# Performance work log

Measured on AMD Instinct MI355X. Metric: run time of the kernel, lower is better.

Reference implementation:

```python
import jax, jax.numpy as jnp
import numpy as np

B, S, H, NH, DIS = 8, 512, 512, 8, 32
HD = H // NH  # head_dim = 64


def setup_inputs() -> dict:
    key = jax.random.key(0)
    ks = jax.random.split(key, 9)
    sc = 0.05
    return {
        "x": jax.random.normal(ks[0], (B, S, H), jnp.float32),
        "rel_distance": jax.random.randint(ks[1], (B, S, 2 * S), 0, DIS, jnp.int64),
        "mask": jnp.zeros((B, S, 2 * S), jnp.bool_),
        "query_pos_embedding": jax.random.normal(ks[2], (DIS, H), jnp.float32) * sc,
        "key_pos_embedding": jax.random.normal(ks[3], (DIS, H), jnp.float32) * sc,
        "value_pos_embedding": jax.random.normal(ks[4], (DIS, H), jnp.float32) * sc,
        "Wq": jax.random.normal(ks[5], (H, H), jnp.float32) * sc,
        "Wk": jax.random.normal(ks[6], (2 * H, H), jnp.float32) * sc,
        "Wv": jax.random.normal(ks[7], (2 * H, H), jnp.float32) * sc,
        "Wo": jax.random.normal(ks[8], (H, H), jnp.float32) * sc,
    }


def reference(x, rel_distance, mask, query_pos_embedding, key_pos_embedding,
              value_pos_embedding, Wq, Wk, Wv, Wo):
    b, s, _ = x.shape
    scale = jnp.sqrt(jnp.asarray(HD, x.dtype))

    # projections (torch Linear: y = x @ W.T)
    q = (x @ Wq.T).reshape(b, s, NH, HD).transpose(0, 2, 1, 3)        # [B,h,S,d]
    k = (x @ Wk.T).reshape(b, 2 * s, NH, HD).transpose(0, 2, 1, 3)    # [B,h,2S,d]
    v = (x @ Wv.T).reshape(b, 2 * s, NH, HD).transpose(0, 2, 1, 3)    # [B,h,2S,d]

    rel = jnp.broadcast_to(rel_distance[:, None], (b, NH, s, 2 * s))  # [B,h,S,2S]

    # relative-position weights via gather along distance axis
    q_emb = query_pos_embedding.reshape(DIS, NH, HD)                  # [n,h,d]
    qpw_full = jnp.einsum('bhsd,nhd->bhsn', q, q_emb)                 # [B,h,S,n]
    qpw = jnp.take_along_axis(qpw_full, rel, axis=3)                  # [B,h,S,2S]

    k_emb = key_pos_embedding.reshape(DIS, NH, HD)
    kpw_full = jnp.einsum('bhkd,nhd->bhkn', k, k_emb)                 # [B,h,2S,n]
    kpw = jnp.take_along_axis(kpw_full, rel.transpose(0, 1, 3, 2), axis=3)  # [B,h,2S,S]
    kpw = kpw.transpose(0, 1, 3, 2)                                   # [B,h,S,2S]

    scores = (jnp.einsum('bhsd,bhkd->bhsk', q, k) + qpw + kpw) / scale
    scores = jnp.where(mask[:, None], -jnp.inf, scores)
    probs = jax.nn.softmax(scores, axis=-1)                           # [B,h,S,2S]

    # scatter-add probs into distance buckets: [B,h,S,n]
    bi = jnp.arange(b)[:, None, None, None]
    hi = jnp.arange(NH)[None, :, None, None]
    si = jnp.arange(s)[None, None, :, None]
    vdw = jnp.zeros((b, NH, s, DIS), probs.dtype).at[bi, hi, si, rel].add(probs)

    v_emb = value_pos_embedding.reshape(DIS, NH, HD)                  # [n,h,d]
    out = jnp.einsum('bhsk,bhkd->bhsd', probs, v) \
        + jnp.einsum('bhsn,nhd->bhsd', vdw, v_emb)                    # [B,h,S,d]
    out = out.transpose(0, 2, 1, 3).reshape(b, s, H)
    return out @ Wo.T
```

## Files before the change

kernel.cpp:

```cpp
#include <hip/hip_runtime.h>
#include <math.h>

#define Bc 8
#define Sc 512
#define Hc 512
#define NHc 8
#define HDc 64
#define DISc 32
#define S2c 1024

typedef __attribute__((ext_vector_type(8))) short bf16x8;
typedef __attribute__((ext_vector_type(4))) float f32x4;
#define MFMA16(a, b, c) __builtin_amdgcn_mfma_f32_16x16x32_bf16(a, b, c, 0, 0, 0)

__device__ __forceinline__ unsigned short f2bf(float f) {
  unsigned u = __float_as_uint(f);
  return (unsigned short)((u + 0x7fffu + ((u >> 16) & 1u)) >> 16);
}
__device__ __forceinline__ float b2f(unsigned short u) {
  return __uint_as_float((unsigned)u << 16);
}
__device__ __forceinline__ bf16x8 ldb16x8(const unsigned short* p) {
  union { uint4 u; bf16x8 s; } cv;
  cv.u = *(const uint4*)p;
  return cv.s;
}

__global__ __launch_bounds__(256) void cvt5_k(
    const float* __restrict__ x, const float* __restrict__ wq,
    const float* __restrict__ wk, const float* __restrict__ wv,
    const float* __restrict__ wo, unsigned short* __restrict__ x16,
    unsigned short* __restrict__ w16q, unsigned short* __restrict__ w16k,
    unsigned short* __restrict__ w16v, unsigned short* __restrict__ w16o) {
  int i = blockIdx.x * 256 + threadIdx.x;
  const float* src; unsigned short* dst; int off; float sc = 1.f;
  if (i < 524288)      { src = x;  dst = x16;  off = i; }
  else if (i < 589824) { src = wq; dst = w16q; off = i - 524288; sc = 0.125f; }
  else if (i < 720896) { src = wk; dst = w16k; off = i - 589824; }
  else if (i < 851968) { src = wv; dst = w16v; off = i - 720896; }
  else                 { src = wo; dst = w16o; off = i - 851968; }
  float4 v = ((const float4*)src)[off];
  ushort4 u;
  u.x = f2bf(v.x * sc); u.y = f2bf(v.y * sc);
  u.z = f2bf(v.z * sc); u.w = f2bf(v.w * sc);
  ((ushort4*)dst)[off] = u;
}

__global__ __launch_bounds__(256) void pack_k(const int* __restrict__ rel,
                                              const unsigned char* __restrict__ mask,
                                              unsigned char* __restrict__ pk8) {
  int i = blockIdx.x * 256 + threadIdx.x;
  const int* rp = rel + i * 16;
  uint4 mu = *(const uint4*)(mask + i * 16);
  const unsigned char* mb = (const unsigned char*)&mu;
  uint4 o;
  unsigned* ow = (unsigned*)&o;
#pragma unroll
  for (int g = 0; g < 4; ++g) {
    int4 r4 = ((const int4*)rp)[g];
    unsigned b0 = ((unsigned)r4.x & 31u) | (mb[g * 4 + 0] ? 0x80u : 0u);
    unsigned b1 = ((unsigned)r4.y & 31u) | (mb[g * 4 + 1] ? 0x80u : 0u);
    unsigned b2 = ((unsigned)r4.z & 31u) | (mb[g * 4 + 2] ? 0x80u : 0u);
    unsigned b3 = ((unsigned)r4.w & 31u) | (mb[g * 4 + 3] ? 0x80u : 0u);
    ow[g] = b0 | (b1 << 8) | (b2 << 16) | (b3 << 24);
  }
  *(uint4*)(pk8 + i * 16) = o;
}

__global__ __launch_bounds__(256) void wemb_k(
    const float* __restrict__ qpe, const float* __restrict__ kpe,
    const float* __restrict__ Wq, const float* __restrict__ Wk,
    unsigned short* __restrict__ wqp, unsigned short* __restrict__ wkp) {
  const int bid = blockIdx.x;
  const int cc = bid & 3, unit = bid >> 2;
  const int c0 = cc << 7;
  const int t = threadIdx.x;
  const float* emb; const float* Wsrc; unsigned short* outp; int rowbase, h;
  if (unit < 8) {
    h = unit; emb = qpe; Wsrc = Wq + (size_t)(h * 64) * 512; outp = wqp; rowbase = h * 32;
  } else {
    int u = unit - 8; int e = u >> 3; h = u & 7;
    emb = kpe; Wsrc = Wk + (size_t)(e * 512 + h * 64) * 512; outp = wkp;
    rowbase = e * 256 + h * 32;
  }
  __shared__ float es[32][65];
  __shared__ float wsh[64][132];
  {
    int n = t >> 3, d4 = (t & 7) << 3;
    float4 v0 = *(const float4*)(emb + (size_t)n * 512 + h * 64 + d4);
    float4 v1 = *(const float4*)(emb + (size_t)n * 512 + h * 64 + d4 + 4);
    *(float4*)&es[n][d4] = v0;
    *(float4*)&es[n][d4 + 4] = v1;
  }
#pragma unroll
  for (int p = 0; p < 8; ++p) {
    int slot = t + (p << 8);
    int d = slot >> 5, c4 = (slot & 31) << 2;
    *(float4*)&wsh[d][c4] = *(const float4*)(Wsrc + (size_t)d * 512 + c0 + c4);
  }
  __syncthreads();
  const int n = t >> 3, cb = (t & 7) << 4;
  float acc[16] = {};
#pragma unroll
  for (int d = 0; d < 64; ++d) {
    float ev = es[n][d];
    float4 w0 = *(const float4*)&wsh[d][cb];
    float4 w1 = *(const float4*)&wsh[d][cb + 4];
    float4 w2 = *(const float4*)&wsh[d][cb + 8];
    float4 w3 = *(const float4*)&wsh[d][cb + 12];
    acc[0] = fmaf(ev, w0.x, acc[0]);   acc[1] = fmaf(ev, w0.y, acc[1]);
    acc[2] = fmaf(ev, w0.z, acc[2]);   acc[3] = fmaf(ev, w0.w, acc[3]);
    acc[4] = fmaf(ev, w1.x, acc[4]);   acc[5] = fmaf(ev, w1.y, acc[5]);
    acc[6] = fmaf(ev, w1.z, acc[6]);   acc[7] = fmaf(ev, w1.w, acc[7]);
    acc[8] = fmaf(ev, w2.x, acc[8]);   acc[9] = fmaf(ev, w2.y, acc[9]);
    acc[10] = fmaf(ev, w2.z, acc[10]); acc[11] = fmaf(ev, w2.w, acc[11]);
    acc[12] = fmaf(ev, w3.x, acc[12]); acc[13] = fmaf(ev, w3.y, acc[13]);
    acc[14] = fmaf(ev, w3.z, acc[14]); acc[15] = fmaf(ev, w3.w, acc[15]);
  }
  unsigned short* orow = outp + (size_t)(rowbase + n) * 512 + c0 + cb;
#pragma unroll
  for (int j = 0; j < 16; ++j) orow[j] = f2bf(acc[j] * 0.125f);
}

template <int MODE>
__global__ __launch_bounds__(256, 4) void gemm16_k(
    const unsigned short* __restrict__ A, const unsigned short* __restrict__ B1,
    const unsigned short* __restrict__ B2, void* __restrict__ out1,
    void* __restrict__ out2, int M, int N, int K, int nsplit) {
  const int t = threadIdx.x;
  const int w = t >> 6, lane = t & 63, ln = lane & 15, qd = lane >> 4;
  const int wm = (w >> 1) << 5, wn = (w & 1) << 5;
  const int m0 = blockIdx.y << 6, n0 = blockIdx.x << 6;
  __shared__ unsigned short As[64 * 72];
  __shared__ unsigned short Bs[64 * 72];
  const bool reg1 = (n0 < nsplit);
  const unsigned short* Bb =
      reg1 ? B1 + (size_t)n0 * K : B2 + (size_t)(n0 - nsplit) * K;
  const int r0 = t >> 3, c8 = (t & 7) << 3;
  const unsigned short* ga = A + (size_t)(m0 + r0) * K + c8;
  const unsigned short* gb = Bb + (size_t)r0 * K + c8;
  const size_t half = (size_t)32 * K;
  uint4 va0 = *(const uint4*)ga, va1 = *(const uint4*)(ga + half);
  uint4 vb0 = *(const uint4*)gb, vb1 = *(const uint4*)(gb + half);
  f32x4 z = {0.f, 0.f, 0.f, 0.f};
  f32x4 acc[2][2] = {{z, z}, {z, z}};
  for (int k0 = 0; k0 < K; k0 += 64) {
    *(uint4*)&As[r0 * 72 + c8] = va0;
    *(uint4*)&As[(r0 + 32) * 72 + c8] = va1;
    *(uint4*)&Bs[r0 * 72 + c8] = vb0;
    *(uint4*)&Bs[(r0 + 32) * 72 + c8] = vb1;
    __syncthreads();
    if (k0 + 64 < K) {
      va0 = *(const uint4*)(ga + k0 + 64);
      va1 = *(const uint4*)(ga + half + k0 + 64);
      vb0 = *(const uint4*)(gb + k0 + 64);
      vb1 = *(const uint4*)(gb + half + k0 + 64);
    }
#pragma unroll
    for (int kk = 0; kk < 64; kk += 32) {
      bf16x8 a0 = ldb16x8(&As[(wm + ln) * 72 + kk + qd * 8]);
      bf16x8 a1 = ldb16x8(&As[(wm + 16 + ln) * 72 + kk + qd * 8]);
      bf16x8 b0 = ldb16x8(&Bs[(wn + ln) * 72 + kk + qd * 8]);
      bf16x8 b1 = ldb16x8(&Bs[(wn + 16 + ln) * 72 + kk + qd * 8]);
      acc[0][0] = MFMA16(a0, b0, acc[0][0]);
      acc[0][1] = MFMA16(a0, b1, acc[0][1]);
      acc[1][0] = MFMA16(a1, b0, acc[1][0]);
      acc[1][1] = MFMA16(a1, b1, acc[1][1]);
    }
    __syncthreads();
  }
#pragma unroll
  for (int tm = 0; tm < 2; ++tm)
#pragma unroll
    for (int tn = 0; tn < 2; ++tn)
#pragma unroll
      for (int r = 0; r < 4; ++r) {
        int m = m0 + wm + tm * 16 + qd * 4 + r;
        int n = n0 + wn + tn * 16 + ln;
        float v = acc[tm][tn][r];
        int bb = m >> 9, s = m & 511;
        if (MODE == 0) {
          ((float*)out1)[(size_t)m * N + n] = v;
        } else if (MODE == 3) {
          int e = n >> 9, hh = (n >> 6) & 7, d = n & 63;
          int k2 = 2 * s + e;
          ((unsigned short*)out1)[((size_t)(bb * 8 + hh) * 64 + d) * 1024 + k2] = f2bf(v);
        } else if (MODE == 1) {
          if (reg1) {
            int hh = (n >> 6) & 7, d = n & 63;
            ((unsigned short*)out1)[((size_t)(bb * 8 + hh) * 512 + s) * 64 + d] = f2bf(v);
          } else {
            int n2 = n - 512, hh = n2 >> 5, nn = n2 & 31;
            ((unsigned short*)out2)[((size_t)(bb * 8 + hh) * 512 + s) * 32 + nn] = f2bf(v);
          }
        } else {
          if (reg1) {
            int e = n >> 9, hh = (n >> 6) & 7, d = n & 63;
            int k2 = 2 * s + e;
            ((unsigned short*)out1)[((size_t)(bb * 8 + hh) * 1024 + k2) * 64 + d] = f2bf(v);
          } else {
            int n2 = n - 1024, e = n2 >> 8, hh = (n2 >> 5) & 7, nn = n2 & 31;
            int k2 = 2 * s + e;
            ((unsigned short*)out2)[((size_t)(bb * 8 + hh) * 1024 + k2) * 32 + nn] = f2bf(v);
          }
        }
      }
}

__global__ __launch_bounds__(512, 4) void attn6_k(
    const unsigned short* __restrict__ q16h, const unsigned short* __restrict__ kb16,
    const unsigned short* __restrict__ vT16, const unsigned short* __restrict__ qpw16,
    const unsigned short* __restrict__ kpw16, const unsigned char* __restrict__ pk8,
    const float* __restrict__ v_emb, unsigned short* __restrict__ attn16) {
  const int bid = blockIdx.x;
  const int b = bid & 7;
  const int h = (bid >> 3) & 7;
  const int qb = ((bid >> 6) & 7) << 6;
  const int t = threadIdx.x;
  const int w = t >> 6;
  const int g = w >> 2;
  const int ws4 = w & 3;
  const int lane = t & 63;
  const int ln = lane & 15;
  const int qd = lane >> 4;

  __shared__ __align__(16) char smem[60928];
  unsigned char*  pkt  = (unsigned char*)smem;
  unsigned short* kpws = (unsigned short*)(smem + 10240);
  unsigned short* q32s = (unsigned short*)(smem + 19456);
  unsigned short* pbuf = (unsigned short*)(smem + 24064);
  unsigned long long* vdwm64 = (unsigned long long*)(smem + 42496);
  float*          accbuf = (float*)smem;
  unsigned short* vest   = (unsigned short*)(smem + 24064);
  unsigned short* vdwb   = (unsigned short*)(smem + 29184);

  for (int i = t; i < 4 * 16 * 36; i += 512) vdwm64[i] = 0ull;
  if (t < 256) {
    int row = t >> 2, c8 = (t & 3) << 3;
    *(uint4*)&q32s[row * 36 + c8] =
        *(const uint4*)(qpw16 + ((size_t)((b * 8 + h) * 512 + qb) + row) * 32 + c8);
  }
  const unsigned short* kbase = kb16 + (size_t)(b * 8 + h) * 65536;
  const unsigned short* vbase = vT16 + (size_t)(b * 8 + h) * 65536;
  bf16x8 aQ[2];
  {
    const unsigned short* qsrc =
        q16h + ((size_t)((b * 8 + h) * 512 + qb + ws4 * 16 + ln)) * 64;
    aQ[0] = ldb16x8(qsrc + qd * 8);
    aQ[1] = ldb16x8(qsrc + 32 + qd * 8);
  }
  f32x4 z = {0.f, 0.f, 0.f, 0.f};
  f32x4 acc[4] = {z, z, z, z};

  const int u = t & 255, gg = t >> 8;
  const int qr = u >> 2, cg = (u & 3) << 4;
  const int kc8 = (u & 3) << 3;
  const unsigned char* pks = pk8 + ((size_t)(b * 512 + qb + qr)) * 1024 + (gg << 9);
  const unsigned short* kps =
      kpw16 + ((size_t)((b * 8 + h) * 1024) + (gg << 9) + qr) * 32 + kc8;
  unsigned char* pt_w = pkt + gg * 5120 + qr * 80 + cg;
  unsigned short* kp_w = kpws + gg * 2304 + qr * 36 + kc8;

  uint4 pv = *(const uint4*)(pks + cg);
  uint4 kv = *(const uint4*)kps;

  for (int kti = 0; kti < 8; ++kti) {
    *(uint4*)pt_w = pv;
    *(uint4*)kp_w = kv;
    __syncthreads();
    if (kti < 7) {
      pv = *(const uint4*)(pks + ((kti + 1) << 6) + cg);
      kv = *(const uint4*)(kps + ((size_t)(kti + 1) << 11));
    }
    const int kt0 = (kti + g * 8) << 6;

    f32x4 sc4[4];
#pragma unroll
    for (int t4 = 0; t4 < 4; ++t4) {
      f32x4 c = z;
      c = MFMA16(aQ[0], ldb16x8(kbase + (size_t)(kt0 + t4 * 16 + ln) * 64 + qd * 8), c);
      c = MFMA16(aQ[1], ldb16x8(kbase + (size_t)(kt0 + t4 * 16 + ln) * 64 + 32 + qd * 8), c);
      sc4[t4] = c;
    }

    unsigned char* pt_ = pkt + g * 5120;
    unsigned short* kp_ = kpws + g * 2304;
#pragma unroll
    for (int r = 0; r < 4; ++r) {
#pragma unroll
      for (int t4 = 0; t4 < 4; ++t4) {
        int row_l = ws4 * 16 + qd * 4 + r;
        int kl = t4 * 16 + ln;
        unsigned um = pt_[row_l * 80 + kl];
        int rd = um & 31;
        float s = sc4[t4][r] + b2f(q32s[row_l * 36 + rd]) + b2f(kp_[kl * 36 + rd]);
        float p = (um & 0x80u) ? 0.f : __expf(s);
        atomicAdd(&vdwm64[ws4 * 576 + (qd * 4 + r) * 36 + rd],
                  (unsigned long long)(p * 67108864.0f));
        pbuf[w * 1152 + (qd * 4 + r) * 72 + kl] = f2bf(p);
      }
    }

    bf16x8 a0 = ldb16x8(&pbuf[w * 1152 + ln * 72 + qd * 8]);
    bf16x8 a1 = ldb16x8(&pbuf[w * 1152 + ln * 72 + 32 + qd * 8]);
#pragma unroll
    for (int dt = 0; dt < 4; ++dt) {
      acc[dt] = MFMA16(a0, ldb16x8(vbase + (size_t)(dt * 16 + ln) * 1024 + kt0 + qd * 8), acc[dt]);
      acc[dt] = MFMA16(a1, ldb16x8(vbase + (size_t)(dt * 16 + ln) * 1024 + kt0 + 32 + qd * 8), acc[dt]);
    }
    __syncthreads();
  }

  if (t < 256) {
    int n = t >> 3, d0 = (t & 7) << 3;
    const float* src = v_emb + ((size_t)n << 9) + (h << 6) + d0;
    float4 f0 = *(const float4*)src;
    float4 f1 = *(const float4*)(src + 4);
    vest[(d0 + 0) * 40 + n] = f2bf(f0.x); vest[(d0 + 1) * 40 + n] = f2bf(f0.y);
    vest[(d0 + 2) * 40 + n] = f2bf(f0.z); vest[(d0 + 3) * 40 + n] = f2bf(f0.w);
    vest[(d0 + 4) * 40 + n] = f2bf(f1.x); vest[(d0 + 5) * 40 + n] = f2bf(f1.y);
    vest[(d0 + 6) * 40 + n] = f2bf(f1.z); vest[(d0 + 7) * 40 + n] = f2bf(f1.w);
  } else {
    int row = lane >> 2, n0 = (lane & 3) << 3;
    float vv[8];
#pragma unroll
    for (int j = 0; j < 8; ++j)
      vv[j] = (float)vdwm64[ws4 * 576 + row * 36 + n0 + j] * 1.4901161193847656e-8f;
    ushort4 u0, u1;
    u0.x = f2bf(vv[0]); u0.y = f2bf(vv[1]); u0.z = f2bf(vv[2]); u0.w = f2bf(vv[3]);
    u1.x = f2bf(vv[4]); u1.y = f2bf(vv[5]); u1.z = f2bf(vv[6]); u1.w = f2bf(vv[7]);
    *(ushort4*)&vdwb[ws4 * 640 + row * 40 + n0] = u0;
    *(ushort4*)&vdwb[ws4 * 640 + row * 40 + n0 + 4] = u1;
  }
  __syncthreads();

  if (g == 1) {
    bf16x8 av = ldb16x8(&vdwb[ws4 * 640 + ln * 40 + qd * 8]);
#pragma unroll
    for (int dt = 0; dt < 4; ++dt)
      acc[dt] = MFMA16(av, ldb16x8(&vest[(dt * 16 + ln) * 40 + qd * 8]), acc[dt]);
#pragma unroll
    for (int r = 0; r < 4; ++r)
#pragma unroll
      for (int dt = 0; dt < 4; ++dt)
        accbuf[ws4 * 1088 + (qd * 4 + r) * 68 + dt * 16 + ln] = acc[dt][r];
  }
  __syncthreads();

  if (g == 0) {
    float inv[4];
#pragma unroll
    for (int r = 0; r < 4; ++r) {
      unsigned long long lu = 0ull;
#pragma unroll
      for (int n = 0; n < 32; ++n)
        lu += vdwm64[ws4 * 576 + (qd * 4 + r) * 36 + n];
      inv[r] = 67108864.0f / (float)lu;
    }
    unsigned short* obase =
        attn16 + ((size_t)(b * 512 + qb + ws4 * 16 + qd * 4)) * 512 + (h << 6);
#pragma unroll
    for (int r = 0; r < 4; ++r)
#pragma unroll
      for (int dt = 0; dt < 4; ++dt) {
        float v = (acc[dt][r] + accbuf[ws4 * 1088 + (qd * 4 + r) * 68 + dt * 16 + ln]) * inv[r];
        obase[(size_t)r * 512 + dt * 16 + ln] = f2bf(v);
      }
  }
}

extern "C" void kernel_launch(void* const* d_in, const int* in_sizes, int n_in,
                              void* d_out, int out_size, void* d_ws, size_t ws_size,
                              hipStream_t stream) {
  const float* x = (const float*)d_in[0];
  const int* rel = (const int*)d_in[1];
  const unsigned char* mask = (const unsigned char*)d_in[2];
  const float* qpe = (const float*)d_in[3];
  const float* kpe = (const float*)d_in[4];
  const float* vpe = (const float*)d_in[5];
  const float* Wq = (const float*)d_in[6];
  const float* Wk = (const float*)d_in[7];
  const float* Wv = (const float*)d_in[8];
  const float* Wo = (const float*)d_in[9];
  float* out = (float*)d_out;

  unsigned short* u = (unsigned short*)d_ws;
  unsigned short* x16    = u;
  unsigned short* w16q   = x16 + 2097152;
  unsigned short* w16k   = w16q + 262144;
  unsigned short* w16v   = w16k + 524288;
  unsigned short* w16o   = w16v + 524288;
  unsigned short* wqp16  = w16o + 262144;
  unsigned short* wkp16  = wqp16 + 131072;
  unsigned short* q16h   = wkp16 + 262144;
  unsigned short* qpw16  = q16h + 2097152;
  unsigned short* kb16   = qpw16 + 1048576;
  unsigned short* kpw16  = kb16 + 4194304;
  unsigned short* vT16   = kpw16 + 2097152;
  unsigned short* attn16 = vT16 + 4194304;
  unsigned char* pk8 = (unsigned char*)(attn16 + 2097152);

  pack_k<<<1024, 256, 0, stream>>>(rel, mask, pk8);
  cvt5_k<<<3584, 256, 0, stream>>>(x, Wq, Wk, Wv, Wo, x16, w16q, w16k, w16v, w16o);
  wemb_k<<<96, 256, 0, stream>>>(qpe, kpe, Wq, Wk, wqp16, wkp16);
  gemm16_k<1><<<dim3(12, 64), 256, 0, stream>>>(x16, w16q, wqp16, q16h, qpw16,
                                                4096, 768, 512, 512);
  gemm16_k<2><<<dim3(24, 64), 256, 0, stream>>>(x16, w16k, wkp16, kb16, kpw16,
                                                4096, 1536, 512, 1024);
  gemm16_k<3><<<dim3(16, 64), 256, 0, stream>>>(x16, w16v, nullptr, vT16, nullptr,
                                                4096, 1024, 512, 1024);
  attn6_k<<<512, 512, 0, stream>>>(q16h, kb16, vT16, qpw16, kpw16, pk8, vpe, attn16);
  gemm16_k<0><<<dim3(8, 64), 256, 0, stream>>>(attn16, w16o, nullptr, out, nullptr,
                                               4096, 512, 512, 512);
}
```

Baseline: 221.2 us.

## Use direct global-to-LDS loads and 128x64 tiles in bf16 GEMM

The projection and output GEMMs now stage tiles with global_load_lds, which copies global memory straight into LDS instead of going through registers, and the block tile grows from 64x64 to 128x64 with four row-fragments per wave. The goal is less register traffic for staging and more MFMA reuse per LDS fragment load. The cost is that the register prefetch of the next K tile is gone, the LDS padding is dropped (which may cause bank conflicts on fragment reads), and the grids launch half as many blocks.

```diff
diff --git a/kernel.cpp b/kernel.cpp
--- a/kernel.cpp
+++ b/kernel.cpp
@@ -24,6 +24,11 @@
   union { uint4 u; bf16x8 s; } cv;
   cv.u = *(const uint4*)p;
   return cv.s;
+}
+__device__ __forceinline__ void gll16(const unsigned short* g, void* l) {
+  __builtin_amdgcn_global_load_lds(
+      (const __attribute__((address_space(1))) unsigned int*)g,
+      (__attribute__((address_space(3))) unsigned int*)l, 16, 0, 0);
 }
 
 __global__ __launch_bounds__(256) void cvt5_k(
@@ -129,48 +134,47 @@
     void* __restrict__ out2, int M, int N, int K, int nsplit) {
   const int t = threadIdx.x;
   const int w = t >> 6, lane = t & 63, ln = lane & 15, qd = lane >> 4;
-  const int wm = (w >> 1) << 5, wn = (w & 1) << 5;
-  const int m0 = blockIdx.y << 6, n0 = blockIdx.x << 6;
-  __shared__ unsigned short As[64 * 72];
-  __shared__ unsigned short Bs[64 * 72];
+  const int wm = (w >> 1) << 6, wn = (w & 1) << 5;
+  const int m0 = blockIdx.y << 7, n0 = blockIdx.x << 6;
+  __shared__ __align__(16) unsigned short As[128 * 64];
+  __shared__ __align__(16) unsigned short Bs[64 * 64];
   const bool reg1 = (n0 < nsplit);
   const unsigned short* Bb =
       reg1 ? B1 + (size_t)n0 * K : B2 + (size_t)(n0 - nsplit) * K;
-  const int r0 = t >> 3, c8 = (t & 7) << 3;
-  const unsigned short* ga = A + (size_t)(m0 + r0) * K + c8;
-  const unsigned short* gb = Bb + (size_t)r0 * K + c8;
-  const size_t half = (size_t)32 * K;
-  uint4 va0 = *(const uint4*)ga, va1 = *(const uint4*)(ga + half);
-  uint4 vb0 = *(const uint4*)gb, vb1 = *(const uint4*)(gb + half);
+  const int lr = lane >> 3, lc = (lane & 7) << 3;
+  const unsigned short* ga = A + (size_t)(m0 + (w << 5) + lr) * K + lc;
+  const unsigned short* gb = Bb + (size_t)((w << 4) + lr) * K + lc;
+  char* lA = (char*)As + (w << 12);
+  char* lB = (char*)Bs + (w << 11);
   f32x4 z = {0.f, 0.f, 0.f, 0.f};
-  f32x4 acc[2][2] = {{z, z}, {z, z}};
+  f32x4 acc[4][2] = {{z, z}, {z, z}, {z, z}, {z, z}};
   for (int k0 = 0; k0 < K; k0 += 64) {
-    *(uint4*)&As[r0 * 72 + c8] = va0;
-    *(uint4*)&As[(r0 + 32) * 72 + c8] = va1;
-    *(uint4*)&Bs[r0 * 72 + c8] = vb0;
-    *(uint4*)&Bs[(r0 + 32) * 72 + c8] = vb1;
+#pragma unroll
+    for (int i = 0; i < 4; ++i)
+      gll16(ga + (size_t)(i << 3) * K + k0, lA + (i << 10));
+#pragma unroll
+    for (int i = 0; i < 2; ++i)
+      gll16(gb + (size_t)(i << 3) * K + k0, lB + (i << 10));
     __syncthreads();
-    if (k0 + 64 < K) {
-      va0 = *(const uint4*)(ga + k0 + 64);
-      va1 = *(const uint4*)(ga + half + k0 + 64);
-      vb0 = *(const uint4*)(gb + k0 + 64);
-      vb1 = *(const uint4*)(gb + half + k0 + 64);
-    }
 #pragma unroll
     for (int kk = 0; kk < 64; kk += 32) {
-      bf16x8 a0 = ldb16x8(&As[(wm + ln) * 72 + kk + qd * 8]);
-      bf16x8 a1 = ldb16x8(&As[(wm + 16 + ln) * 72 + kk + qd * 8]);
-      bf16x8 b0 = ldb16x8(&Bs[(wn + ln) * 72 + kk + qd * 8]);
-      bf16x8 b1 = ldb16x8(&Bs[(wn + 16 + ln) * 72 + kk + qd * 8]);
-      acc[0][0] = MFMA16(a0, b0, acc[0][0]);
-      acc[0][1] = MFMA16(a0, b1, acc[0][1]);
-      acc[1][0] = MFMA16(a1, b0, acc[1][0]);
-      acc[1][1] = MFMA16(a1, b1, acc[1][1]);
+      bf16x8 af[4], bfr[2];
+#pragma unroll
+      for (int x = 0; x < 4; ++x)
+        af[x] = ldb16x8(&As[(wm + x * 16 + ln) * 64 + kk + qd * 8]);
+#pragma unroll
+      for (int y = 0; y < 2; ++y)
+        bfr[y] = ldb16x8(&Bs[(wn + y * 16 + ln) * 64 + kk + qd * 8]);
+#pragma unroll
+      for (int tm = 0; tm < 4; ++tm)
+#pragma unroll
+        for (int tn = 0; tn < 2; ++tn)
+          acc[tm][tn] = MFMA16(af[tm], bfr[tn], acc[tm][tn]);
     }
     __syncthreads();
   }
 #pragma unroll
-  for (int tm = 0; tm < 2; ++tm)
+  for (int tm = 0; tm < 4; ++tm)
 #pragma unroll
     for (int tn = 0; tn < 2; ++tn)
 #pragma unroll
@@ -403,13 +407,13 @@
   pack_k<<<1024, 256, 0, stream>>>(rel, mask, pk8);
   cvt5_k<<<3584, 256, 0, stream>>>(x, Wq, Wk, Wv, Wo, x16, w16q, w16k, w16v, w16o);
   wemb_k<<<96, 256, 0, stream>>>(qpe, kpe, Wq, Wk, wqp16, wkp16);
-  gemm16_k<1><<<dim3(12, 64), 256, 0, stream>>>(x16, w16q, wqp16, q16h, qpw16,
+  gemm16_k<1><<<dim3(12, 32), 256, 0, stream>>>(x16, w16q, wqp16, q16h, qpw16,
                                                 4096, 768, 512, 512);
-  gemm16_k<2><<<dim3(24, 64), 256, 0, stream>>>(x16, w16k, wkp16, kb16, kpw16,
+  gemm16_k<2><<<dim3(24, 32), 256, 0, stream>>>(x16, w16k, wkp16, kb16, kpw16,
                                                 4096, 1536, 512, 1024);
-  gemm16_k<3><<<dim3(16, 64), 256, 0, stream>>>(x16, w16v, nullptr, vT16, nullptr,
+  gemm16_k<3><<<dim3(16, 32), 256, 0, stream>>>(x16, w16v, nullptr, vT16, nullptr,
                                                 4096, 1024, 512, 1024);
   attn6_k<<<512, 512, 0, stream>>>(q16h, kb16, vT16, qpw16, kpw16, pk8, vpe, attn16);
-  gemm16_k<0><<<dim3(8, 64), 256, 0, stream>>>(attn16, w16o, nullptr, out, nullptr,
+  gemm16_k<0><<<dim3(8, 32), 256, 0, stream>>>(attn16, w16o, nullptr, out, nullptr,
                                                4096, 512, 512, 512);
 }
```

After: 231.0 us. 1.04x slower.

## Merge Q/K/V projection GEMMs into one launch and shrink attention P buffer

Applied to the files above, without the earlier changes.

The three projection GEMM launches (Q+qpw, K+kpw, V transposed) become one kernel over a 52-column-tile grid that selects the weight source and output layout per tile. This removes two launch gaps and gives one larger wave of blocks. The attention kernel now handles the P·V product in two 32-key halves, so the per-wave probability buffer shrinks and total LDS drops. Launch bounds rise to 6 blocks per SM to raise occupancy, which may cost registers or spill.

```diff
diff --git a/kernel.cpp b/kernel.cpp
--- a/kernel.cpp
+++ b/kernel.cpp
@@ -122,35 +122,41 @@
   for (int j = 0; j < 16; ++j) orow[j] = f2bf(acc[j] * 0.125f);
 }
 
-template <int MODE>
-__global__ __launch_bounds__(256, 4) void gemm16_k(
-    const unsigned short* __restrict__ A, const unsigned short* __restrict__ B1,
-    const unsigned short* __restrict__ B2, void* __restrict__ out1,
-    void* __restrict__ out2, int M, int N, int K, int nsplit) {
+__global__ __launch_bounds__(256, 4) void gemmqkv_k(
+    const unsigned short* __restrict__ A,
+    const unsigned short* __restrict__ wq, const unsigned short* __restrict__ wqp,
+    const unsigned short* __restrict__ wk, const unsigned short* __restrict__ wkp,
+    const unsigned short* __restrict__ wv,
+    unsigned short* __restrict__ q16h, unsigned short* __restrict__ qpw16,
+    unsigned short* __restrict__ kb16, unsigned short* __restrict__ kpw16,
+    unsigned short* __restrict__ vT16) {
   const int t = threadIdx.x;
   const int w = t >> 6, lane = t & 63, ln = lane & 15, qd = lane >> 4;
   const int wm = (w >> 1) << 5, wn = (w & 1) << 5;
   const int m0 = blockIdx.y << 6, n0 = blockIdx.x << 6;
   __shared__ unsigned short As[64 * 72];
   __shared__ unsigned short Bs[64 * 72];
-  const bool reg1 = (n0 < nsplit);
-  const unsigned short* Bb =
-      reg1 ? B1 + (size_t)n0 * K : B2 + (size_t)(n0 - nsplit) * K;
+  const unsigned short* Bb;
+  if (n0 < 512)        Bb = wq  + (size_t)n0 * 512;
+  else if (n0 < 768)   Bb = wqp + (size_t)(n0 - 512) * 512;
+  else if (n0 < 1792)  Bb = wk  + (size_t)(n0 - 768) * 512;
+  else if (n0 < 2304)  Bb = wkp + (size_t)(n0 - 1792) * 512;
+  else                 Bb = wv  + (size_t)(n0 - 2304) * 512;
   const int r0 = t >> 3, c8 = (t & 7) << 3;
-  const unsigned short* ga = A + (size_t)(m0 + r0) * K + c8;
-  const unsigned short* gb = Bb + (size_t)r0 * K + c8;
-  const size_t half = (size_t)32 * K;
+  const unsigned short* ga = A + (size_t)(m0 + r0) * 512 + c8;
+  const unsigned short* gb = Bb + (size_t)r0 * 512 + c8;
+  const size_t half = (size_t)32 * 512;
   uint4 va0 = *(const uint4*)ga, va1 = *(const uint4*)(ga + half);
   uint4 vb0 = *(const uint4*)gb, vb1 = *(const uint4*)(gb + half);
   f32x4 z = {0.f, 0.f, 0.f, 0.f};
   f32x4 acc[2][2] = {{z, z}, {z, z}};
-  for (int k0 = 0; k0 < K; k0 += 64) {
+  for (int k0 = 0; k0 < 512; k0 += 64) {
     *(uint4*)&As[r0 * 72 + c8] = va0;
     *(uint4*)&As[(r0 + 32) * 72 + c8] = va1;
     *(uint4*)&Bs[r0 * 72 + c8] = vb0;
     *(uint4*)&Bs[(r0 + 32) * 72 + c8] = vb1;
     __syncthreads();
-    if (k0 + 64 < K) {
+    if (k0 + 64 < 512) {
       va0 = *(const uint4*)(ga + k0 + 64);
       va1 = *(const uint4*)(ga + half + k0 + 64);
       vb0 = *(const uint4*)(gb + k0 + 64);
@@ -177,37 +183,86 @@
       for (int r = 0; r < 4; ++r) {
         int m = m0 + wm + tm * 16 + qd * 4 + r;
         int n = n0 + wn + tn * 16 + ln;
-        float v = acc[tm][tn][r];
+        unsigned short v16 = f2bf(acc[tm][tn][r]);
         int bb = m >> 9, s = m & 511;
-        if (MODE == 0) {
-          ((float*)out1)[(size_t)m * N + n] = v;
-        } else if (MODE == 3) {
-          int e = n >> 9, hh = (n >> 6) & 7, d = n & 63;
+        if (n0 < 512) {
+          int hh = (n >> 6) & 7, d = n & 63;
+          q16h[((size_t)(bb * 8 + hh) * 512 + s) * 64 + d] = v16;
+        } else if (n0 < 768) {
+          int n2 = n - 512, hh = n2 >> 5, nn = n2 & 31;
+          qpw16[((size_t)(bb * 8 + hh) * 512 + s) * 32 + nn] = v16;
+        } else if (n0 < 1792) {
+          int n2 = n - 768, e = n2 >> 9, hh = (n2 >> 6) & 7, d = n2 & 63;
           int k2 = 2 * s + e;
-          ((unsigned short*)out1)[((size_t)(bb * 8 + hh) * 64 + d) * 1024 + k2] = f2bf(v);
-        } else if (MODE == 1) {
-          if (reg1) {
-            int hh = (n >> 6) & 7, d = n & 63;
-            ((unsigned short*)out1)[((size_t)(bb * 8 + hh) * 512 + s) * 64 + d] = f2bf(v);
-          } else {
-            int n2 = n - 512, hh = n2 >> 5, nn = n2 & 31;
-            ((unsigned short*)out2)[((size_t)(bb * 8 + hh) * 512 + s) * 32 + nn] = f2bf(v);
-          }
+          kb16[((size_t)(bb * 8 + hh) * 1024 + k2) * 64 + d] = v16;
+        } else if (n0 < 2304) {
+          int n2 = n - 1792, e = n2 >> 8, hh = (n2 >> 5) & 7, nn = n2 & 31;
+          int k2 = 2 * s + e;
+          kpw16[((size_t)(bb * 8 + hh) * 1024 + k2) * 32 + nn] = v16;
         } else {
-          if (reg1) {
-            int e = n >> 9, hh = (n >> 6) & 7, d = n & 63;
-            int k2 = 2 * s + e;
-            ((unsigned short*)out1)[((size_t)(bb * 8 + hh) * 1024 + k2) * 64 + d] = f2bf(v);
-          } else {
-            int n2 = n - 1024, e = n2 >> 8, hh = (n2 >> 5) & 7, nn = n2 & 31;
-            int k2 = 2 * s + e;
-            ((unsigned short*)out2)[((size_t)(bb * 8 + hh) * 1024 + k2) * 32 + nn] = f2bf(v);
-          }
+          int n2 = n - 2304, e = n2 >> 9, hh = (n2 >> 6) & 7, d = n2 & 63;
+          int k2 = 2 * s + e;
+          vT16[((size_t)(bb * 8 + hh) * 64 + d) * 1024 + k2] = v16;
         }
       }
 }
 
-__global__ __launch_bounds__(512, 4) void attn6_k(
+__global__ __launch_bounds__(256, 4) void gemmo_k(
+    const unsigned short* __restrict__ A, const unsigned short* __restrict__ Bw,
+    float* __restrict__ out) {
+  const int t = threadIdx.x;
+  const int w = t >> 6, lane = t & 63, ln = lane & 15, qd = lane >> 4;
+  const int wm = (w >> 1) << 5, wn = (w & 1) << 5;
+  const int m0 = blockIdx.y << 6, n0 = blockIdx.x << 6;
+  __shared__ unsigned short As[64 * 72];
+  __shared__ unsigned short Bs[64 * 72];
+  const unsigned short* Bb = Bw + (size_t)n0 * 512;
+  const int r0 = t >> 3, c8 = (t & 7) << 3;
+  const unsigned short* ga = A + (size_t)(m0 + r0) * 512 + c8;
+  const unsigned short* gb = Bb + (size_t)r0 * 512 + c8;
+  const size_t half = (size_t)32 * 512;
+  uint4 va0 = *(const uint4*)ga, va1 = *(const uint4*)(ga + half);
+  uint4 vb0 = *(const uint4*)gb, vb1 = *(const uint4*)(gb + half);
+  f32x4 z = {0.f, 0.f, 0.f, 0.f};
+  f32x4 acc[2][2] = {{z, z}, {z, z}};
+  for (int k0 = 0; k0 < 512; k0 += 64) {
+    *(uint4*)&As[r0 * 72 + c8] = va0;
+    *(uint4*)&As[(r0 + 32) * 72 + c8] = va1;
+    *(uint4*)&Bs[r0 * 72 + c8] = vb0;
+    *(uint4*)&Bs[(r0 + 32) * 72 + c8] = vb1;
+    __syncthreads();
+    if (k0 + 64 < 512) {
+      va0 = *(const uint4*)(ga + k0 + 64);
+      va1 = *(const uint4*)(ga + half + k0 + 64);
+      vb0 = *(const uint4*)(gb + k0 + 64);
+      vb1 = *(const uint4*)(gb + half + k0 + 64);
+    }
+#pragma unroll
+    for (int kk = 0; kk < 64; kk += 32) {
+      bf16x8 a0 = ldb16x8(&As[(wm + ln) * 72 + kk + qd * 8]);
+      bf16x8 a1 = ldb16x8(&As[(wm + 16 + ln) * 72 + kk + qd * 8]);
+      bf16x8 b0 = ldb16x8(&Bs[(wn + ln) * 72 + kk + qd * 8]);
+      bf16x8 b1 = ldb16x8(&Bs[(wn + 16 + ln) * 72 + kk + qd * 8]);
+      acc[0][0] = MFMA16(a0, b0, acc[0][0]);
+      acc[0][1] = MFMA16(a0, b1, acc[0][1]);
+      acc[1][0] = MFMA16(a1, b0, acc[1][0]);
+      acc[1][1] = MFMA16(a1, b1, acc[1][1]);
+    }
+    __syncthreads();
+  }
+#pragma unroll
+  for (int tm = 0; tm < 2; ++tm)
+#pragma unroll
+    for (int tn = 0; tn < 2; ++tn)
+#pragma unroll
+      for (int r = 0; r < 4; ++r) {
+        int m = m0 + wm + tm * 16 + qd * 4 + r;
+        int n = n0 + wn + tn * 16 + ln;
+        out[(size_t)m * 512 + n] = acc[tm][tn][r];
+      }
+}
+
+__global__ __launch_bounds__(512, 6) void attn6_k(
     const unsigned short* __restrict__ q16h, const unsigned short* __restrict__ kb16,
     const unsigned short* __restrict__ vT16, const unsigned short* __restrict__ qpw16,
     const unsigned short* __restrict__ kpw16, const unsigned char* __restrict__ pk8,
@@ -224,15 +279,15 @@
   const int ln = lane & 15;
   const int qd = lane >> 4;
 
-  __shared__ __align__(16) char smem[60928];
+  __shared__ __align__(16) char smem[52736];
   unsigned char*  pkt  = (unsigned char*)smem;
   unsigned short* kpws = (unsigned short*)(smem + 10240);
   unsigned short* q32s = (unsigned short*)(smem + 19456);
   unsigned short* pbuf = (unsigned short*)(smem + 24064);
-  unsigned long long* vdwm64 = (unsigned long long*)(smem + 42496);
+  unsigned long long* vdwm64 = (unsigned long long*)(smem + 34304);
   float*          accbuf = (float*)smem;
-  unsigned short* vest   = (unsigned short*)(smem + 24064);
-  unsigned short* vdwb   = (unsigned short*)(smem + 29184);
+  unsigned short* vest   = (unsigned short*)(smem + 19456);
+  unsigned short* vdwb   = (unsigned short*)(smem + 24576);
 
   for (int i = t; i < 4 * 16 * 36; i += 512) vdwm64[i] = 0ull;
   if (t < 256) {
@@ -286,27 +341,27 @@
     unsigned char* pt_ = pkt + g * 5120;
     unsigned short* kp_ = kpws + g * 2304;
 #pragma unroll
-    for (int r = 0; r < 4; ++r) {
-#pragma unroll
-      for (int t4 = 0; t4 < 4; ++t4) {
-        int row_l = ws4 * 16 + qd * 4 + r;
-        int kl = t4 * 16 + ln;
-        unsigned um = pt_[row_l * 80 + kl];
-        int rd = um & 31;
-        float s = sc4[t4][r] + b2f(q32s[row_l * 36 + rd]) + b2f(kp_[kl * 36 + rd]);
-        float p = (um & 0x80u) ? 0.f : __expf(s);
-        atomicAdd(&vdwm64[ws4 * 576 + (qd * 4 + r) * 36 + rd],
-                  (unsigned long long)(p * 67108864.0f));
-        pbuf[w * 1152 + (qd * 4 + r) * 72 + kl] = f2bf(p);
+    for (int hf = 0; hf < 2; ++hf) {
+#pragma unroll
+      for (int r = 0; r < 4; ++r) {
+#pragma unroll
+        for (int t4h = 0; t4h < 2; ++t4h) {
+          int t4 = hf * 2 + t4h;
+          int row_l = ws4 * 16 + qd * 4 + r;
+          int kl = t4 * 16 + ln;
+          unsigned um = pt_[row_l * 80 + kl];
+          int rd = um & 31;
+          float s = sc4[t4][r] + b2f(q32s[row_l * 36 + rd]) + b2f(kp_[kl * 36 + rd]);
+          float p = (um & 0x80u) ? 0.f : __expf(s);
+          atomicAdd(&vdwm64[ws4 * 576 + (qd * 4 + r) * 36 + rd],
+                    (unsigned long long)(p * 67108864.0f));
+          pbuf[w * 640 + (qd * 4 + r) * 40 + t4h * 16 + ln] = f2bf(p);
+        }
       }
-    }
-
-    bf16x8 a0 = ldb16x8(&pbuf[w * 1152 + ln * 72 + qd * 8]);
-    bf16x8 a1 = ldb16x8(&pbuf[w * 1152 + ln * 72 + 32 + qd * 8]);
-#pragma unroll
-    for (int dt = 0; dt < 4; ++dt) {
-      acc[dt] = MFMA16(a0, ldb16x8(vbase + (size_t)(dt * 16 + ln) * 1024 + kt0 + qd * 8), acc[dt]);
-      acc[dt] = MFMA16(a1, ldb16x8(vbase + (size_t)(dt * 16 + ln) * 1024 + kt0 + 32 + qd * 8), acc[dt]);
+      bf16x8 ah = ldb16x8(&pbuf[w * 640 + ln * 40 + qd * 8]);
+#pragma unroll
+      for (int dt = 0; dt < 4; ++dt)
+        acc[dt] = MFMA16(ah, ldb16x8(vbase + (size_t)(dt * 16 + ln) * 1024 + kt0 + hf * 32 + qd * 8), acc[dt]);
     }
     __syncthreads();
   }
@@ -403,13 +458,8 @@
   pack_k<<<1024, 256, 0, stream>>>(rel, mask, pk8);
   cvt5_k<<<3584, 256, 0, stream>>>(x, Wq, Wk, Wv, Wo, x16, w16q, w16k, w16v, w16o);
   wemb_k<<<96, 256, 0, stream>>>(qpe, kpe, Wq, Wk, wqp16, wkp16);
-  gemm16_k<1><<<dim3(12, 64), 256, 0, stream>>>(x16, w16q, wqp16, q16h, qpw16,
-                                                4096, 768, 512, 512);
-  gemm16_k<2><<<dim3(24, 64), 256, 0, stream>>>(x16, w16k, wkp16, kb16, kpw16,
-                                                4096, 1536, 512, 1024);
-  gemm16_k<3><<<dim3(16, 64), 256, 0, stream>>>(x16, w16v, nullptr, vT16, nullptr,
-                                                4096, 1024, 512, 1024);
+  gemmqkv_k<<<dim3(52, 64), 256, 0, stream>>>(x16, w16q, wqp16, w16k, wkp16, w16v,
+                                              q16h, qpw16, kb16, kpw16, vT16);
   attn6_k<<<512, 512, 0, stream>>>(q16h, kb16, vT16, qpw16, kpw16, pk8, vpe, attn16);
-  gemm16_k<0><<<dim3(8, 64), 256, 0, stream>>>(attn16, w16o, nullptr, out, nullptr,
-                                               4096, 512, 512, 512);
-}
+  gemmo_k<<<dim3(8, 64), 256, 0, stream>>>(attn16, w16o, out);
+}
```

Result: slower. 255.9 us (+15.6%).
